# Optimization experiments

Measured on AMD Instinct MI355X. Metric: run time of the kernel, lower is better.

The kernel has to match this reference:

```python
import jax, jax.numpy as jnp
import numpy as np

B, S, H = 4, 8192, 768
NH, HD = 12, 64          # num_heads, head_size
M = 64                   # projection_dim = min(256, HD)
EPS = 1e-6

def setup_inputs() -> dict:
    key = jax.random.key(0)
    ks = jax.random.split(key, 10)
    scale_w = 0.02
    scale_p = 1.0 / np.sqrt(HD)
    return {
        'hidden_states': jax.random.normal(ks[0], (B, S, H), jnp.float32),
        'Wq': jax.random.normal(ks[1], (H, H), jnp.float32) * scale_w,
        'bq': jnp.zeros((H,), jnp.float32),
        'Wk': jax.random.normal(ks[2], (H, H), jnp.float32) * scale_w,
        'bk': jnp.zeros((H,), jnp.float32),
        'Wv': jax.random.normal(ks[3], (H, H), jnp.float32) * scale_w,
        'bv': jnp.zeros((H,), jnp.float32),
        'Wo': jax.random.normal(ks[4], (H, H), jnp.float32) * scale_w,
        'bo': jnp.zeros((H,), jnp.float32),
        'projection_matrix': jax.random.normal(ks[5], (NH, HD, M), jnp.float32) * scale_p,
    }

def reference(hidden_states, Wq, bq, Wk, bk, Wv, bv, Wo, bo, projection_matrix):
    b, s, h = hidden_states.shape
    def heads(x):  # [b,s,h] -> [b,nh,s,hd]
        return x.reshape(b, s, NH, HD).transpose(0, 2, 1, 3)
    q = heads(hidden_states @ Wq + bq)
    k = heads(hidden_states @ Wk + bk)
    v = heads(hidden_states @ Wv + bv)
    # random-feature projection + stabilized exp feature map
    qp = jnp.einsum('bhnd,hdm->bhnm', q, projection_matrix)
    kp = jnp.einsum('bhnd,hdm->bhnm', k, projection_matrix)
    qp = jnp.exp(qp - jnp.max(qp, axis=-1, keepdims=True))
    kp = jnp.exp(kp - jnp.max(kp, axis=-1, keepdims=True))
    # O(n) linear attention: kv summary [b,h,m,hd]
    kv = jnp.einsum('bhnm,bhnd->bhmd', kp, v)
    qkv = jnp.einsum('bhnm,bhmd->bhnd', qp, kv)
    k_sum = jnp.sum(kp, axis=2)                      # [b,h,m]
    normalizer = jnp.einsum('bhnm,bhm->bhn', qp, k_sum)[..., None]
    ctx = qkv / (normalizer + EPS)
    ctx = ctx.transpose(0, 2, 1, 3).reshape(b, s, NH * HD)
    return ctx @ Wo + bo
```

## Files before the change

kernel.cpp:

```cpp
#include <hip/hip_runtime.h>
#include <hip/hip_bf16.h>


#define S_    8192
#define H_    768
#define NH_   12
#define EPS_  1e-6f

typedef unsigned short U16;
typedef short bf16x8 __attribute__((ext_vector_type(8)));
typedef float f32x4  __attribute__((ext_vector_type(4)));

__device__ __forceinline__ U16 f2b(float x) {
  unsigned u = __float_as_uint(x);
  return (U16)((u + 0x7fffu + ((u >> 16) & 1u)) >> 16);
}
__device__ __forceinline__ float b2f(U16 h) {
  return __uint_as_float(((unsigned)h) << 16);
}
__device__ __forceinline__ void gl2lds16(const void* g, void* l) {
  __builtin_amdgcn_global_load_lds(
      (const __attribute__((address_space(1))) void*)g,
      (__attribute__((address_space(3))) void*)l, 16, 0, 0);
}

__global__ void zero_f32(float* __restrict__ p, int n) {
  int i = blockIdx.x * 256 + threadIdx.x;
  if (i < n) p[i] = 0.f;
}

__global__ void cvt_f32_bf16(const float* __restrict__ src, U16* __restrict__ hi, int n4) {
  int i = blockIdx.x * 256 + threadIdx.x;
  if (i >= n4) return;
  float4 x = ((const float4*)src)[i];
  ushort4 h;
  h.x = f2b(x.x); h.y = f2b(x.y); h.z = f2b(x.z); h.w = f2b(x.w);
  ((ushort4*)hi)[i] = h;
}

__global__ void fold_proj(const float* __restrict__ Wq, const float* __restrict__ bq,
                          const float* __restrict__ Wk, const float* __restrict__ bk,
                          const float* __restrict__ P,
                          float* __restrict__ Wqp, float* __restrict__ bqp,
                          float* __restrict__ Wkp, float* __restrict__ bkp) {
  __shared__ float Pl[64 * 64];
  __shared__ float WL[4 * 64];
  int h = blockIdx.y, kc = blockIdx.x, tid = threadIdx.x;
  const float* W  = blockIdx.z ? Wk : Wq;
  const float* bb = blockIdx.z ? bk : bq;
  float* Wout = blockIdx.z ? Wkp : Wqp;
  float* bout = blockIdx.z ? bkp : bqp;
  const float4* P4 = (const float4*)(P + (size_t)h * 4096);
#pragma unroll
  for (int i = 0; i < 4; ++i) ((float4*)Pl)[tid + i * 256] = P4[tid + i * 256];
  WL[tid] = W[(size_t)(kc * 4 + (tid >> 6)) * H_ + h * 64 + (tid & 63)];
  __syncthreads();
  int kl = tid >> 6, m = tid & 63;
  float acc = 0.f;
#pragma unroll
  for (int d = 0; d < 64; ++d) acc += WL[kl * 64 + d] * Pl[d * 64 + m];
  Wout[(size_t)(kc * 4 + kl) * H_ + h * 64 + m] = acc;
  if (kc == 0 && tid < 64) {
    float a2 = 0.f;
    for (int d = 0; d < 64; ++d) a2 += bb[h * 64 + d] * Pl[d * 64 + tid];
    bout[h * 64 + tid] = a2;
  }
}

__global__ void build_cat_t(const float* __restrict__ Wqp, const float* __restrict__ Wkp,
                            const float* __restrict__ Wv,  const float* __restrict__ Wo,
                            U16* __restrict__ WcatH, U16* __restrict__ WoTH) {
  __shared__ float T[64][68];
  const int kb = blockIdx.x, rb = blockIdx.y, mat = blockIdx.z;
  const int tid = threadIdx.x;
  const float* W = mat == 0 ? Wqp : (mat == 1 ? Wkp : (mat == 2 ? Wv : Wo));
#pragma unroll
  for (int p = 0; p < 4; ++p) {
    int idx = tid + p * 256;
    int rr = idx >> 4, c4 = (idx & 15) * 4;
    float4 v = *(const float4*)&W[(size_t)(kb * 64 + rr) * H_ + rb * 64 + c4];
    T[rr][c4] = v.x; T[rr][c4 + 1] = v.y; T[rr][c4 + 2] = v.z; T[rr][c4 + 3] = v.w;
  }
  __syncthreads();
  U16* dst = mat == 3 ? WoTH : WcatH;
  const int rbase = (mat == 3 ? 0 : mat * 768) + rb * 64;
#pragma unroll
  for (int p = 0; p < 4; ++p) {
    int idx = tid + p * 256;
    int r2 = idx >> 4, c2 = (idx & 15) * 4;
    ushort4 o;
    o.x = f2b(T[c2 + 0][r2]); o.y = f2b(T[c2 + 1][r2]);
    o.z = f2b(T[c2 + 2][r2]); o.w = f2b(T[c2 + 3][r2]);
    *(ushort4*)&dst[(size_t)(rbase + r2) * H_ + kb * 64 + c2] = o;
  }
}

__global__ void build_bias(const float* __restrict__ bqp, const float* __restrict__ bkp,
                           const float* __restrict__ bv, float* __restrict__ biasC) {
  int i = blockIdx.x * 256 + threadIdx.x;
  if (i >= 2304) return;
  biasC[i] = i < 768 ? bqp[i] : (i < 1536 ? bkp[i - 768] : bv[i - 1536]);
}

__global__ __launch_bounds__(256, 2) void gemm_qkv(
    const U16* __restrict__ Ahi, const U16* __restrict__ Bhi,
    const float* __restrict__ bias,
    U16* __restrict__ qp, U16* __restrict__ kpT, U16* __restrict__ vT,
    float* __restrict__ ksumF) {
  __shared__ __align__(16) U16 Us[32768];
  const int tid = threadIdx.x, w = tid >> 6, lane = tid & 63;
  const int quad = lane >> 4, l16 = lane & 15;
  const int b = blockIdx.x;
  const int mt = b & 255, nt0 = b >> 8;
  const int rowA0 = mt * 128;
  const int wm = w & 1, wn = w >> 1;
  const U16* srcA[4];
  int rowBl[4];
  unsigned ldsc[4];
  const int kch = ((lane & 7) ^ (lane >> 3)) * 8;
#pragma unroll
  for (int t = 0; t < 4; ++t) {
    int c = w * 4 + t;
    int row = c * 8 + (lane >> 3);
    srcA[t] = Ahi + (size_t)(rowA0 + row) * H_ + kch;
    rowBl[t] = row;
    ldsc[t] = (unsigned)c * 512;
  }
  auto stage = [&](int jn, int tn, int bi) {
    const int colB = (nt0 + 2 * jn) * 128;
    unsigned ub = (unsigned)bi * 16384u;
#pragma unroll
    for (int t = 0; t < 4; ++t) {
      gl2lds16(srcA[t] + tn * 64, &Us[ub + ldsc[t]]);
      gl2lds16(Bhi + (size_t)(colB + rowBl[t]) * H_ + tn * 64 + kch,
               &Us[ub + 8192u + ldsc[t]]);
    }
  };

  stage(0, 0, 0);
  for (int jj = 0; jj < 9; ++jj) {
    const int colB0 = (nt0 + 2 * jj) * 128;
    f32x4 acc[4][4] = {};
    for (int t = 0; t < 12; ++t) {
      const bool more = !(jj == 8 && t == 11);
      if (more) {
        if (t < 11) stage(jj, t + 1, (t + 1) & 1);
        else        stage(jj + 1, 0, 0);
        asm volatile("s_waitcnt vmcnt(8)" ::: "memory");
      } else {
        asm volatile("s_waitcnt vmcnt(0)" ::: "memory");
      }
      __builtin_amdgcn_sched_barrier(0);
      __builtin_amdgcn_s_barrier();
      __builtin_amdgcn_sched_barrier(0);
      const unsigned ab = (unsigned)(t & 1) * 16384u;
      bf16x8 ah[4][2], bh[4][2];
#pragma unroll
      for (int i = 0; i < 4; ++i)
#pragma unroll
        for (int ks = 0; ks < 2; ++ks)
          ah[i][ks] = *(const bf16x8*)&Us[ab +
              (unsigned)((wm * 64 + i * 16 + l16) * 64 +
                         (((ks * 4 + quad) ^ (l16 & 7)) * 8))];
#pragma unroll
      for (int j = 0; j < 4; ++j)
#pragma unroll
        for (int ks = 0; ks < 2; ++ks)
          bh[j][ks] = *(const bf16x8*)&Us[ab + 8192u +
              (unsigned)((wn * 64 + j * 16 + l16) * 64 +
                         (((ks * 4 + quad) ^ (l16 & 7)) * 8))];
      asm volatile("s_waitcnt lgkmcnt(0)" ::: "memory");
      __builtin_amdgcn_sched_barrier(0);
      __builtin_amdgcn_s_setprio(1);
#pragma unroll
      for (int ks = 0; ks < 2; ++ks)
#pragma unroll
        for (int j = 0; j < 4; ++j)
#pragma unroll
          for (int i = 0; i < 4; ++i)
            acc[i][j] = __builtin_amdgcn_mfma_f32_16x16x32_bf16(
                ah[i][ks], bh[j][ks], acc[i][j], 0, 0, 0);
      __builtin_amdgcn_s_setprio(0);
      __builtin_amdgcn_sched_barrier(0);
      __builtin_amdgcn_s_barrier();
      __builtin_amdgcn_sched_barrier(0);
    }
    const int col64 = colB0 + wn * 64;
    float bj[4];
#pragma unroll
    for (int j = 0; j < 4; ++j) bj[j] = bias[col64 + j * 16 + l16];
    if (col64 < 768) {
      const int h = col64 >> 6;
#pragma unroll
      for (int i = 0; i < 4; ++i) {
#pragma unroll
        for (int r = 0; r < 4; ++r) {
          int row = rowA0 + wm * 64 + i * 16 + quad * 4 + r;
          float v0 = acc[i][0][r] + bj[0], v1 = acc[i][1][r] + bj[1];
          float v2 = acc[i][2][r] + bj[2], v3 = acc[i][3][r] + bj[3];
          float mx = fmaxf(fmaxf(v0, v1), fmaxf(v2, v3));
          mx = fmaxf(mx, __shfl_xor(mx, 1));
          mx = fmaxf(mx, __shfl_xor(mx, 2));
          mx = fmaxf(mx, __shfl_xor(mx, 4));
          mx = fmaxf(mx, __shfl_xor(mx, 8));
          int bb = row >> 13, s = row & 8191;
          size_t base = ((size_t)(bb * NH_ + h) * S_ + s) * 64 + l16;
          qp[base +  0] = f2b(__expf(v0 - mx));
          qp[base + 16] = f2b(__expf(v1 - mx));
          qp[base + 32] = f2b(__expf(v2 - mx));
          qp[base + 48] = f2b(__expf(v3 - mx));
        }
      }
    } else {
      const int isv = col64 >= 1536;
      const int h = (col64 - (isv ? 1536 : 768)) >> 6;
      U16* dstT = isv ? vT : kpT;
      const int bh2 = (rowA0 >> 13) * NH_ + h;
      float pk[4] = {0.f, 0.f, 0.f, 0.f};
#pragma unroll
      for (int i = 0; i < 4; ++i) {
        float er[4][4];
#pragma unroll
        for (int r = 0; r < 4; ++r) {
          float v0 = acc[i][0][r] + bj[0], v1 = acc[i][1][r] + bj[1];
          float v2 = acc[i][2][r] + bj[2], v3 = acc[i][3][r] + bj[3];
          if (!isv) {
            float mx = fmaxf(fmaxf(v0, v1), fmaxf(v2, v3));
            mx = fmaxf(mx, __shfl_xor(mx, 1));
            mx = fmaxf(mx, __shfl_xor(mx, 2));
            mx = fmaxf(mx, __shfl_xor(mx, 4));
            mx = fmaxf(mx, __shfl_xor(mx, 8));
            v0 = __expf(v0 - mx); v1 = __expf(v1 - mx);
            v2 = __expf(v2 - mx); v3 = __expf(v3 - mx);
          }
          er[0][r] = v0; er[1][r] = v1; er[2][r] = v2; er[3][r] = v3;
        }
        if (!isv) {
#pragma unroll
          for (int j = 0; j < 4; ++j)
            pk[j] += er[j][0] + er[j][1] + er[j][2] + er[j][3];
        }
        int n = rowA0 + wm * 64 + i * 16 + quad * 4;
        int s = n & 8191;
#pragma unroll
        for (int j = 0; j < 4; ++j) {
          ushort4 o;
          o.x = f2b(er[j][0]); o.y = f2b(er[j][1]);
          o.z = f2b(er[j][2]); o.w = f2b(er[j][3]);
          *(ushort4*)&dstT[((size_t)bh2 * 64 + j * 16 + l16) * S_ + s] = o;
        }
      }
      if (!isv) {
#pragma unroll
        for (int j = 0; j < 4; ++j) {
          pk[j] += __shfl_xor(pk[j], 16);
          pk[j] += __shfl_xor(pk[j], 32);
        }
        if (quad == 0) {
#pragma unroll
          for (int j = 0; j < 4; ++j)
            atomicAdd(&ksumF[bh2 * 64 + j * 16 + l16], pk[j]);
        }
      }
    }
  }
}

__global__ __launch_bounds__(256, 4) void kv_accum_mfma(
    const U16* __restrict__ kpT, const U16* __restrict__ vT,
    float* __restrict__ kvM) {
  __shared__ __align__(16) U16 Us[2 * 64 * 64];
  const int tid = threadIdx.x, w = tid >> 6, lane = tid & 63;
  const int quad = lane >> 4, l16 = lane & 15;
  const int bh = blockIdx.y;
  const int n0 = blockIdx.x * 512;
  const U16* srcs[4];
  unsigned ldsoff[4];
#pragma unroll
  for (int t = 0; t < 4; ++t) {
    int c = w * 4 + t, buf = c >> 3;
    int r = (c & 7) * 8 + (lane >> 3);
    const U16* base = buf ? kpT : vT;
    srcs[t] = base + ((size_t)bh * 64 + r) * S_ + n0 + (lane & 7) * 8;
    ldsoff[t] = buf * 4096 + (c & 7) * 512;
  }
  f32x4 acc[4] = {};
  for (int nc = 0; nc < 512; nc += 64) {
#pragma unroll
    for (int t = 0; t < 4; ++t) gl2lds16(srcs[t] + nc, &Us[ldsoff[t]]);
    __syncthreads();
#pragma unroll
    for (int k0 = 0; k0 < 64; k0 += 32) {
      bf16x8 av = *(const bf16x8*)&Us[(w * 16 + l16) * 64 + k0 + quad * 8];
#pragma unroll
      for (int j = 0; j < 4; ++j) {
        bf16x8 bk = *(const bf16x8*)&Us[4096 + (j * 16 + l16) * 64 + k0 + quad * 8];
        acc[j] = __builtin_amdgcn_mfma_f32_16x16x32_bf16(av, bk, acc[j], 0, 0, 0);
      }
    }
    __syncthreads();
  }
#pragma unroll
  for (int j = 0; j < 4; ++j)
#pragma unroll
    for (int r = 0; r < 4; ++r)
      atomicAdd(&kvM[((size_t)bh * 64 + j * 16 + l16) * 64 + w * 16 + quad * 4 + r],
                acc[j][r]);
}

__global__ __launch_bounds__(256) void wkv_build(
    const float* __restrict__ kvM, const U16* __restrict__ WoTH,
    U16* __restrict__ WKVT) {
  __shared__ float kvL[64][65];
  __shared__ U16  WoL[128][66];
  const int tid = threadIdx.x;
  const int cB = blockIdx.x * 128, bh = blockIdx.y;
  const int b = bh / NH_, h = bh - b * NH_;
#pragma unroll
  for (int p = 0; p < 16; ++p) {
    int idx = tid + p * 256;
    kvL[idx >> 6][idx & 63] = kvM[(size_t)bh * 4096 + idx];
  }
#pragma unroll
  for (int p = 0; p < 32; ++p) {
    int idx = tid + p * 256;
    WoL[idx >> 6][idx & 63] = WoTH[(size_t)(cB + (idx >> 6)) * H_ + h * 64 + (idx & 63)];
  }
  __syncthreads();
  const int c = tid & 127, m0 = (tid >> 7) * 32;
  float acc[32] = {};
  for (int d = 0; d < 64; ++d) {
    float wv = b2f(WoL[c][d]);
#pragma unroll
    for (int mm = 0; mm < 32; ++mm) acc[mm] += wv * kvL[m0 + mm][d];
  }
  U16* dst = WKVT + (size_t)b * 589824 + (size_t)(cB + c) * H_ + h * 64 + m0;
#pragma unroll
  for (int mm = 0; mm < 32; mm += 4) {
    ushort4 o;
    o.x = f2b(acc[mm]); o.y = f2b(acc[mm + 1]);
    o.z = f2b(acc[mm + 2]); o.w = f2b(acc[mm + 3]);
    *(ushort4*)&dst[mm] = o;
  }
}

__global__ __launch_bounds__(256) void qpn_scale(
    U16* __restrict__ qp, const float* __restrict__ ksumF) {
  __shared__ float ks[64];
  const int tid = threadIdx.x;
  const int bh = blockIdx.y, s0 = blockIdx.x * 64;
  if (tid < 64) ks[tid] = ksumF[bh * 64 + tid];
  __syncthreads();
  const int row = tid >> 2, q = tid & 3;
  size_t src = ((size_t)bh * S_ + s0 + row) * 64 + q * 16;
  bf16x8 x0 = *(const bf16x8*)&qp[src];
  bf16x8 x1 = *(const bf16x8*)&qp[src + 8];
  float f[16];
  float n = 0.f;
#pragma unroll
  for (int e = 0; e < 8; ++e) {
    f[e] = b2f((U16)x0[e]);     n += f[e] * ks[q * 16 + e];
    f[e + 8] = b2f((U16)x1[e]); n += f[e + 8] * ks[q * 16 + 8 + e];
  }
  n += __shfl_xor(n, 1);
  n += __shfl_xor(n, 2);
  const float inv = 1.f / (n + EPS_);
#pragma unroll
  for (int g = 0; g < 4; ++g) {
    ushort4 o;
    o.x = f2b(f[g * 4 + 0] * inv); o.y = f2b(f[g * 4 + 1] * inv);
    o.z = f2b(f[g * 4 + 2] * inv); o.w = f2b(f[g * 4 + 3] * inv);
    *(ushort4*)&qp[src + g * 4] = o;
  }
}

__global__ __launch_bounds__(256, 2) void out_gemm(
    const U16* __restrict__ qpn, const U16* __restrict__ WKVT,
    const float* __restrict__ bo, float* __restrict__ out) {
  __shared__ __align__(16) U16 Us[32768];
  const int tid = threadIdx.x, w = tid >> 6, lane = tid & 63;
  const int quad = lane >> 4, l16 = lane & 15;
  const int b = blockIdx.x;
  const int mt = b & 255, nt0 = b >> 8;
  const int rowA0 = mt * 128;
  const int batch = mt >> 6, s0 = (mt & 63) * 128;
  const int bh0 = batch * NH_;
  const int wm = w & 1, wn = w >> 1;
  const int kch = ((lane & 7) ^ (lane >> 3)) * 8;
  int rowc[4];
  unsigned ldsc[4];
#pragma unroll
  for (int t = 0; t < 4; ++t) {
    rowc[t] = (w * 4 + t) * 8 + (lane >> 3);
    ldsc[t] = (unsigned)(w * 4 + t) * 512;
  }
  const U16* wb = WKVT + (size_t)batch * 589824;
  auto stage = [&](int jn, int tn, int bi) {
    const int colB = (nt0 * 3 + jn) * 128;
    unsigned ub = (unsigned)bi * 16384u;
    const U16* abase = qpn + ((size_t)(bh0 + tn) * S_ + s0) * 64 + kch;
    const U16* bbase = wb + (size_t)colB * H_ + tn * 64 + kch;
#pragma unroll
    for (int t = 0; t < 4; ++t) {
      gl2lds16(abase + rowc[t] * 64, &Us[ub + ldsc[t]]);
      gl2lds16(bbase + (size_t)rowc[t] * H_, &Us[ub + 8192u + ldsc[t]]);
    }
  };

  stage(0, 0, 0);
  for (int jj = 0; jj < 3; ++jj) {
    const int colB0 = (nt0 * 3 + jj) * 128;
    f32x4 acc[4][4] = {};
    for (int t = 0; t < 12; ++t) {
      const bool more = !(jj == 2 && t == 11);
      if (more) {
        if (t < 11) stage(jj, t + 1, (t + 1) & 1);
        else        stage(jj + 1, 0, 0);
        asm volatile("s_waitcnt vmcnt(8)" ::: "memory");
      } else {
        asm volatile("s_waitcnt vmcnt(0)" ::: "memory");
      }
      __builtin_amdgcn_sched_barrier(0);
      __builtin_amdgcn_s_barrier();
      __builtin_amdgcn_sched_barrier(0);
      const unsigned ab = (unsigned)(t & 1) * 16384u;
      bf16x8 ah[4][2], bh[4][2];
#pragma unroll
      for (int i = 0; i < 4; ++i)
#pragma unroll
        for (int ks = 0; ks < 2; ++ks)
          ah[i][ks] = *(const bf16x8*)&Us[ab +
              (unsigned)((wm * 64 + i * 16 + l16) * 64 +
                         (((ks * 4 + quad) ^ (l16 & 7)) * 8))];
#pragma unroll
      for (int j = 0; j < 4; ++j)
#pragma unroll
        for (int ks = 0; ks < 2; ++ks)
          bh[j][ks] = *(const bf16x8*)&Us[ab + 8192u +
              (unsigned)((wn * 64 + j * 16 + l16) * 64 +
                         (((ks * 4 + quad) ^ (l16 & 7)) * 8))];
      asm volatile("s_waitcnt lgkmcnt(0)" ::: "memory");
      __builtin_amdgcn_sched_barrier(0);
      __builtin_amdgcn_s_setprio(1);
#pragma unroll
      for (int ks = 0; ks < 2; ++ks)
#pragma unroll
        for (int j = 0; j < 4; ++j)
#pragma unroll
          for (int i = 0; i < 4; ++i)
            acc[i][j] = __builtin_amdgcn_mfma_f32_16x16x32_bf16(
                ah[i][ks], bh[j][ks], acc[i][j], 0, 0, 0);
      __builtin_amdgcn_s_setprio(0);
      __builtin_amdgcn_sched_barrier(0);
      __builtin_amdgcn_s_barrier();
      __builtin_amdgcn_sched_barrier(0);
    }
#pragma unroll
    for (int i = 0; i < 4; ++i) {
      int row = rowA0 + wm * 64 + i * 16 + quad * 4;
#pragma unroll
      for (int j = 0; j < 4; ++j) {
        int col = colB0 + wn * 64 + j * 16 + l16;
        float bvv = bo[col];
#pragma unroll
        for (int r = 0; r < 4; ++r)
          out[(size_t)(row + r) * H_ + col] = acc[i][j][r] + bvv;
      }
    }
  }
}

extern "C" void kernel_launch(void* const* d_in, const int* in_sizes, int n_in,
                              void* d_out, int out_size, void* d_ws, size_t ws_size,
                              hipStream_t stream) {
  const float* hs = (const float*)d_in[0];
  const float* Wq = (const float*)d_in[1];
  const float* bq = (const float*)d_in[2];
  const float* Wk = (const float*)d_in[3];
  const float* bk = (const float*)d_in[4];
  const float* Wv = (const float*)d_in[5];
  const float* bv = (const float*)d_in[6];
  const float* Wo = (const float*)d_in[7];
  const float* bo = (const float*)d_in[8];
  const float* P  = (const float*)d_in[9];
  float* out = (float*)d_out;

  char* ws = (char*)d_ws;
  size_t off = 0;
  auto alloc = [&](size_t bytes) -> void* {
    void* p = ws + off;
    off = (off + bytes + 255) & ~(size_t)255;
    return p;
  };
  U16*   hs_hi = (U16*)alloc(50331648);
  float* WqpF  = (float*)alloc(2359296);
  float* WkpF  = (float*)alloc(2359296);
  float* bqpF  = (float*)alloc(3072);
  float* bkpF  = (float*)alloc(3072);
  U16*   WcatH = (U16*)alloc(3538944);
  U16*   WoTH  = (U16*)alloc(1179648);
  float* biasC = (float*)alloc(9216);
  U16*   qp    = (U16*)alloc(50331648);
  U16*   kpT   = (U16*)alloc(50331648);
  U16*   vT    = (U16*)alloc(50331648);
  float* kvM   = (float*)alloc(786432);
  float* ksumF = (float*)alloc(12288);
  U16*   WKVT  = (U16*)alloc(4718592);

  zero_f32<<<dim3(780), dim3(256), 0, stream>>>(kvM, 199680);
  cvt_f32_bf16<<<dim3(24576), dim3(256), 0, stream>>>(hs, hs_hi, 6291456);
  fold_proj<<<dim3(192, 12, 2), dim3(256), 0, stream>>>(Wq, bq, Wk, bk, P, WqpF, bqpF, WkpF, bkpF);
  build_cat_t<<<dim3(12, 12, 4), dim3(256), 0, stream>>>(WqpF, WkpF, Wv, Wo, WcatH, WoTH);
  build_bias<<<dim3(9), dim3(256), 0, stream>>>(bqpF, bkpF, bv, biasC);
  gemm_qkv<<<dim3(512), dim3(256), 0, stream>>>(hs_hi, WcatH, biasC, qp, kpT, vT, ksumF);
  kv_accum_mfma<<<dim3(16, 48), dim3(256), 0, stream>>>(kpT, vT, kvM);
  wkv_build<<<dim3(6, 48), dim3(256), 0, stream>>>(kvM, WoTH, WKVT);
  qpn_scale<<<dim3(128, 48), dim3(256), 0, stream>>>(qp, ksumF);
  out_gemm<<<dim3(512), dim3(256), 0, stream>>>(qp, WKVT, bo, out);
}
```

Baseline: 518.6 us.

## Fuse prologue kernels and merge kv accumulation, Wkv build, and q normalization

Merges zeroing, bf16 conversion, projection folding, weight transposes and bias assembly into a single prologue kernel, with the folded Q/K projection written directly as transposed bf16. Combines kv accumulation, the Wo·kv build and q normalization into one kernel, using a per-head atomic ticket so the last block of each head builds the fused output weight. This removes several launches and an fp32 intermediate, but the Wkv build now runs on only one block per head, which reduces its parallelism.

```diff
diff --git a/kernel.cpp b/kernel.cpp
--- a/kernel.cpp
+++ b/kernel.cpp
@@ -24,66 +24,84 @@
       (__attribute__((address_space(3))) void*)l, 16, 0, 0);
 }
 
-__global__ void zero_f32(float* __restrict__ p, int n) {
-  int i = blockIdx.x * 256 + threadIdx.x;
-  if (i < n) p[i] = 0.f;
-}
-
-__global__ void cvt_f32_bf16(const float* __restrict__ src, U16* __restrict__ hi, int n4) {
-  int i = blockIdx.x * 256 + threadIdx.x;
-  if (i >= n4) return;
-  float4 x = ((const float4*)src)[i];
-  ushort4 h;
-  h.x = f2b(x.x); h.y = f2b(x.y); h.z = f2b(x.z); h.w = f2b(x.w);
-  ((ushort4*)hi)[i] = h;
-}
-
-__global__ void fold_proj(const float* __restrict__ Wq, const float* __restrict__ bq,
-                          const float* __restrict__ Wk, const float* __restrict__ bk,
-                          const float* __restrict__ P,
-                          float* __restrict__ Wqp, float* __restrict__ bqp,
-                          float* __restrict__ Wkp, float* __restrict__ bkp) {
-  __shared__ float Pl[64 * 64];
-  __shared__ float WL[4 * 64];
-  int h = blockIdx.y, kc = blockIdx.x, tid = threadIdx.x;
-  const float* W  = blockIdx.z ? Wk : Wq;
-  const float* bb = blockIdx.z ? bk : bq;
-  float* Wout = blockIdx.z ? Wkp : Wqp;
-  float* bout = blockIdx.z ? bkp : bqp;
-  const float4* P4 = (const float4*)(P + (size_t)h * 4096);
-#pragma unroll
-  for (int i = 0; i < 4; ++i) ((float4*)Pl)[tid + i * 256] = P4[tid + i * 256];
-  WL[tid] = W[(size_t)(kc * 4 + (tid >> 6)) * H_ + h * 64 + (tid & 63)];
-  __syncthreads();
-  int kl = tid >> 6, m = tid & 63;
-  float acc = 0.f;
-#pragma unroll
-  for (int d = 0; d < 64; ++d) acc += WL[kl * 64 + d] * Pl[d * 64 + m];
-  Wout[(size_t)(kc * 4 + kl) * H_ + h * 64 + m] = acc;
-  if (kc == 0 && tid < 64) {
-    float a2 = 0.f;
-    for (int d = 0; d < 64; ++d) a2 += bb[h * 64 + d] * Pl[d * 64 + tid];
-    bout[h * 64 + tid] = a2;
-  }
-}
-
-__global__ void build_cat_t(const float* __restrict__ Wqp, const float* __restrict__ Wkp,
-                            const float* __restrict__ Wv,  const float* __restrict__ Wo,
-                            U16* __restrict__ WcatH, U16* __restrict__ WoTH) {
-  __shared__ float T[64][68];
-  const int kb = blockIdx.x, rb = blockIdx.y, mat = blockIdx.z;
-  const int tid = threadIdx.x;
-  const float* W = mat == 0 ? Wqp : (mat == 1 ? Wkp : (mat == 2 ? Wv : Wo));
+__global__ __launch_bounds__(256) void prologue(
+    const float* __restrict__ hs, const float* __restrict__ Wq,
+    const float* __restrict__ bq, const float* __restrict__ Wk,
+    const float* __restrict__ bk, const float* __restrict__ Wv,
+    const float* __restrict__ bv, const float* __restrict__ Wo,
+    const float* __restrict__ P,
+    U16* __restrict__ hs_hi, U16* __restrict__ WcatH, U16* __restrict__ WoTH,
+    float* __restrict__ biasC, float* __restrict__ zbase) {
+  __shared__ float sm[8192];
+  const int bid = blockIdx.x, tid = threadIdx.x;
+  if (bid < 781) {
+    int i = bid * 256 + tid;
+    if (i < 199728) zbase[i] = 0.f;
+    return;
+  }
+  if (bid < 25357) {
+    int i = (bid - 781) * 256 + tid;
+    float4 x = ((const float4*)hs)[i];
+    ushort4 h;
+    h.x = f2b(x.x); h.y = f2b(x.y); h.z = f2b(x.z); h.w = f2b(x.w);
+    ((ushort4*)hs_hi)[i] = h;
+    return;
+  }
+  if (bid < 25645) {
+    int f = bid - 25357;
+    int z = f / 144, rem = f - z * 144, h = rem / 12, kcB = rem - (rem / 12) * 12;
+    float* Pl = sm;
+    float* WL = sm + 4096;
+    const float* W = z ? Wk : Wq;
+    const float4* P4 = (const float4*)(P + (size_t)h * 4096);
+#pragma unroll
+    for (int p = 0; p < 4; ++p) ((float4*)Pl)[tid + p * 256] = P4[tid + p * 256];
+#pragma unroll
+    for (int p = 0; p < 4; ++p) {
+      int idx = tid + p * 256;
+      int kk = idx >> 4, d4 = (idx & 15) * 4;
+      *(float4*)&WL[kk * 64 + d4] =
+          *(const float4*)&W[(size_t)(kcB * 64 + kk) * H_ + h * 64 + d4];
+    }
+    __syncthreads();
+    const int m = tid & 63, kg = tid >> 6;
+    float acc[16] = {};
+    for (int d = 0; d < 64; ++d) {
+      float pv = Pl[d * 64 + m];
+#pragma unroll
+      for (int k2 = 0; k2 < 16; ++k2) acc[k2] += WL[(kg * 16 + k2) * 64 + d] * pv;
+    }
+    U16* dst = WcatH + (size_t)(z * 768 + h * 64 + m) * H_ + kcB * 64 + kg * 16;
+#pragma unroll
+    for (int k2 = 0; k2 < 16; k2 += 4) {
+      ushort4 o;
+      o.x = f2b(acc[k2]); o.y = f2b(acc[k2 + 1]);
+      o.z = f2b(acc[k2 + 2]); o.w = f2b(acc[k2 + 3]);
+      *(ushort4*)&dst[k2] = o;
+    }
+    if (kcB == 0 && tid < 64) {
+      const float* bb = z ? bk : bq;
+      float a2 = 0.f;
+      for (int d = 0; d < 64; ++d) a2 += bb[h * 64 + d] * Pl[d * 64 + tid];
+      biasC[z * 768 + h * 64 + tid] = a2;
+    }
+    return;
+  }
+  const int isWo = bid >= 25789;
+  int v = bid - (isWo ? 25789 : 25645);
+  int kb = v / 12, rb = v - kb * 12;
+  const float* W = isWo ? Wo : Wv;
+  float (*T)[68] = (float(*)[68])sm;
 #pragma unroll
   for (int p = 0; p < 4; ++p) {
     int idx = tid + p * 256;
     int rr = idx >> 4, c4 = (idx & 15) * 4;
-    float4 v = *(const float4*)&W[(size_t)(kb * 64 + rr) * H_ + rb * 64 + c4];
-    T[rr][c4] = v.x; T[rr][c4 + 1] = v.y; T[rr][c4 + 2] = v.z; T[rr][c4 + 3] = v.w;
+    float4 x = *(const float4*)&W[(size_t)(kb * 64 + rr) * H_ + rb * 64 + c4];
+    T[rr][c4] = x.x; T[rr][c4 + 1] = x.y; T[rr][c4 + 2] = x.z; T[rr][c4 + 3] = x.w;
   }
   __syncthreads();
-  U16* dst = mat == 3 ? WoTH : WcatH;
-  const int rbase = (mat == 3 ? 0 : mat * 768) + rb * 64;
+  U16* dst = isWo ? WoTH : WcatH;
+  const int rbase = (isWo ? 0 : 1536) + rb * 64;
 #pragma unroll
   for (int p = 0; p < 4; ++p) {
     int idx = tid + p * 256;
@@ -93,13 +111,10 @@
     o.z = f2b(T[c2 + 2][r2]); o.w = f2b(T[c2 + 3][r2]);
     *(ushort4*)&dst[(size_t)(rbase + r2) * H_ + kb * 64 + c2] = o;
   }
-}
-
-__global__ void build_bias(const float* __restrict__ bqp, const float* __restrict__ bkp,
-                           const float* __restrict__ bv, float* __restrict__ biasC) {
-  int i = blockIdx.x * 256 + threadIdx.x;
-  if (i >= 2304) return;
-  biasC[i] = i < 768 ? bqp[i] : (i < 1536 ? bkp[i - 768] : bv[i - 1536]);
+  if (!isWo && kb == 0 && rb == 0) {
+#pragma unroll
+    for (int p = 0; p < 3; ++p) biasC[1536 + tid + p * 256] = bv[tid + p * 256];
+  }
 }
 
 __global__ __launch_bounds__(256, 2) void gemm_qkv(
@@ -266,89 +281,103 @@
   }
 }
 
-__global__ __launch_bounds__(256, 4) void kv_accum_mfma(
+__global__ __launch_bounds__(256, 2) void kv_qpn(
     const U16* __restrict__ kpT, const U16* __restrict__ vT,
-    float* __restrict__ kvM) {
-  __shared__ __align__(16) U16 Us[2 * 64 * 64];
-  const int tid = threadIdx.x, w = tid >> 6, lane = tid & 63;
-  const int quad = lane >> 4, l16 = lane & 15;
-  const int bh = blockIdx.y;
-  const int n0 = blockIdx.x * 512;
-  const U16* srcs[4];
-  unsigned ldsoff[4];
-#pragma unroll
-  for (int t = 0; t < 4; ++t) {
-    int c = w * 4 + t, buf = c >> 3;
-    int r = (c & 7) * 8 + (lane >> 3);
-    const U16* base = buf ? kpT : vT;
-    srcs[t] = base + ((size_t)bh * 64 + r) * S_ + n0 + (lane & 7) * 8;
-    ldsoff[t] = buf * 4096 + (c & 7) * 512;
-  }
-  f32x4 acc[4] = {};
-  for (int nc = 0; nc < 512; nc += 64) {
-#pragma unroll
-    for (int t = 0; t < 4; ++t) gl2lds16(srcs[t] + nc, &Us[ldsoff[t]]);
+    float* __restrict__ kvM, const float* __restrict__ ksumF,
+    unsigned* __restrict__ tick, const U16* __restrict__ WoTH,
+    U16* __restrict__ WKVT, U16* __restrict__ qp) {
+  __shared__ __align__(16) U16 Us[8192];
+  __shared__ int lastf;
+  const int bid = blockIdx.x, tid = threadIdx.x;
+  if (bid < 768) {
+    const int w = tid >> 6, lane = tid & 63;
+    const int quad = lane >> 4, l16 = lane & 15;
+    const int bh = bid >> 4;
+    const int n0 = (bid & 15) * 512;
+    const U16* srcs[4];
+    unsigned ldsoff[4];
+#pragma unroll
+    for (int t = 0; t < 4; ++t) {
+      int c = w * 4 + t, buf = c >> 3;
+      int r = (c & 7) * 8 + (lane >> 3);
+      const U16* base = buf ? kpT : vT;
+      srcs[t] = base + ((size_t)bh * 64 + r) * S_ + n0 + (lane & 7) * 8;
+      ldsoff[t] = buf * 4096 + (c & 7) * 512;
+    }
+    f32x4 acc[4] = {};
+    for (int nc = 0; nc < 512; nc += 64) {
+#pragma unroll
+      for (int t = 0; t < 4; ++t) gl2lds16(srcs[t] + nc, &Us[ldsoff[t]]);
+      __syncthreads();
+#pragma unroll
+      for (int k0 = 0; k0 < 64; k0 += 32) {
+        bf16x8 av = *(const bf16x8*)&Us[(w * 16 + l16) * 64 + k0 + quad * 8];
+#pragma unroll
+        for (int j = 0; j < 4; ++j) {
+          bf16x8 bk = *(const bf16x8*)&Us[4096 + (j * 16 + l16) * 64 + k0 + quad * 8];
+          acc[j] = __builtin_amdgcn_mfma_f32_16x16x32_bf16(av, bk, acc[j], 0, 0, 0);
+        }
+      }
+      __syncthreads();
+    }
+#pragma unroll
+    for (int j = 0; j < 4; ++j)
+#pragma unroll
+      for (int r = 0; r < 4; ++r)
+        atomicAdd(&kvM[((size_t)bh * 64 + j * 16 + l16) * 64 + w * 16 + quad * 4 + r],
+                  acc[j][r]);
+    __threadfence();
     __syncthreads();
-#pragma unroll
-    for (int k0 = 0; k0 < 64; k0 += 32) {
-      bf16x8 av = *(const bf16x8*)&Us[(w * 16 + l16) * 64 + k0 + quad * 8];
-#pragma unroll
-      for (int j = 0; j < 4; ++j) {
-        bf16x8 bk = *(const bf16x8*)&Us[4096 + (j * 16 + l16) * 64 + k0 + quad * 8];
-        acc[j] = __builtin_amdgcn_mfma_f32_16x16x32_bf16(av, bk, acc[j], 0, 0, 0);
-      }
-    }
+    if (tid == 0) lastf = (atomicAdd(&tick[bh], 1u) == 15u) ? 1 : 0;
     __syncthreads();
-  }
-#pragma unroll
-  for (int j = 0; j < 4; ++j)
-#pragma unroll
-    for (int r = 0; r < 4; ++r)
-      atomicAdd(&kvM[((size_t)bh * 64 + j * 16 + l16) * 64 + w * 16 + quad * 4 + r],
-                acc[j][r]);
-}
-
-__global__ __launch_bounds__(256) void wkv_build(
-    const float* __restrict__ kvM, const U16* __restrict__ WoTH,
-    U16* __restrict__ WKVT) {
-  __shared__ float kvL[64][65];
-  __shared__ U16  WoL[128][66];
-  const int tid = threadIdx.x;
-  const int cB = blockIdx.x * 128, bh = blockIdx.y;
-  const int b = bh / NH_, h = bh - b * NH_;
-#pragma unroll
-  for (int p = 0; p < 16; ++p) {
-    int idx = tid + p * 256;
-    kvL[idx >> 6][idx & 63] = kvM[(size_t)bh * 4096 + idx];
-  }
-#pragma unroll
-  for (int p = 0; p < 32; ++p) {
-    int idx = tid + p * 256;
-    WoL[idx >> 6][idx & 63] = WoTH[(size_t)(cB + (idx >> 6)) * H_ + h * 64 + (idx & 63)];
-  }
-  __syncthreads();
-  const int c = tid & 127, m0 = (tid >> 7) * 32;
-  float acc[32] = {};
-  for (int d = 0; d < 64; ++d) {
-    float wv = b2f(WoL[c][d]);
-#pragma unroll
-    for (int mm = 0; mm < 32; ++mm) acc[mm] += wv * kvL[m0 + mm][d];
-  }
-  U16* dst = WKVT + (size_t)b * 589824 + (size_t)(cB + c) * H_ + h * 64 + m0;
-#pragma unroll
-  for (int mm = 0; mm < 32; mm += 4) {
-    ushort4 o;
-    o.x = f2b(acc[mm]); o.y = f2b(acc[mm + 1]);
-    o.z = f2b(acc[mm + 2]); o.w = f2b(acc[mm + 3]);
-    *(ushort4*)&dst[mm] = o;
-  }
-}
-
-__global__ __launch_bounds__(256) void qpn_scale(
-    U16* __restrict__ qp, const float* __restrict__ ksumF) {
-  __shared__ float ks[64];
-  const int tid = threadIdx.x;
-  const int bh = blockIdx.y, s0 = blockIdx.x * 64;
+    if (!lastf) return;
+    __threadfence();
+    float* kvL = (float*)Us;
+#pragma unroll
+    for (int p = 0; p < 16; ++p) {
+      int i = tid + p * 256;
+      kvL[i] = kvM[(size_t)bh * 4096 + i];
+    }
+    __syncthreads();
+    const int b = bh / NH_, h = bh - b * NH_;
+    for (int cc = 0; cc < 3; ++cc) {
+      int c = tid + cc * 256;
+      const U16* wr = WoTH + (size_t)c * H_ + h * 64;
+#pragma unroll
+      for (int mc = 0; mc < 4; ++mc) {
+        float a16[16] = {};
+#pragma unroll
+        for (int dg = 0; dg < 4; ++dg) {
+          ushort4 w0 = *(const ushort4*)&wr[dg * 16 + 0];
+          ushort4 w1 = *(const ushort4*)&wr[dg * 16 + 4];
+          ushort4 w2 = *(const ushort4*)&wr[dg * 16 + 8];
+          ushort4 w3 = *(const ushort4*)&wr[dg * 16 + 12];
+          U16 wv16[16] = {w0.x, w0.y, w0.z, w0.w, w1.x, w1.y, w1.z, w1.w,
+                          w2.x, w2.y, w2.z, w2.w, w3.x, w3.y, w3.z, w3.w};
+#pragma unroll
+          for (int dd = 0; dd < 16; ++dd) {
+            float wv = b2f(wv16[dd]);
+            int d = dg * 16 + dd;
+#pragma unroll
+            for (int mm = 0; mm < 16; ++mm)
+              a16[mm] += wv * kvL[(mc * 16 + mm) * 64 + d];
+          }
+        }
+        U16* dst = WKVT + (size_t)b * 589824 + (size_t)c * H_ + h * 64 + mc * 16;
+#pragma unroll
+        for (int mm = 0; mm < 16; mm += 4) {
+          ushort4 o;
+          o.x = f2b(a16[mm]); o.y = f2b(a16[mm + 1]);
+          o.z = f2b(a16[mm + 2]); o.w = f2b(a16[mm + 3]);
+          *(ushort4*)&dst[mm] = o;
+        }
+      }
+    }
+    return;
+  }
+  const int qid = bid - 768;
+  const int bh = qid >> 7, s0 = (qid & 127) * 64;
+  float* ks = (float*)Us;
   if (tid < 64) ks[tid] = ksumF[bh * 64 + tid];
   __syncthreads();
   const int row = tid >> 2, q = tid & 3;
@@ -493,10 +522,6 @@
     return p;
   };
   U16*   hs_hi = (U16*)alloc(50331648);
-  float* WqpF  = (float*)alloc(2359296);
-  float* WkpF  = (float*)alloc(2359296);
-  float* bqpF  = (float*)alloc(3072);
-  float* bkpF  = (float*)alloc(3072);
   U16*   WcatH = (U16*)alloc(3538944);
   U16*   WoTH  = (U16*)alloc(1179648);
   float* biasC = (float*)alloc(9216);
@@ -505,16 +530,12 @@
   U16*   vT    = (U16*)alloc(50331648);
   float* kvM   = (float*)alloc(786432);
   float* ksumF = (float*)alloc(12288);
+  unsigned* tick = (unsigned*)alloc(192);
   U16*   WKVT  = (U16*)alloc(4718592);
 
-  zero_f32<<<dim3(780), dim3(256), 0, stream>>>(kvM, 199680);
-  cvt_f32_bf16<<<dim3(24576), dim3(256), 0, stream>>>(hs, hs_hi, 6291456);
-  fold_proj<<<dim3(192, 12, 2), dim3(256), 0, stream>>>(Wq, bq, Wk, bk, P, WqpF, bqpF, WkpF, bkpF);
-  build_cat_t<<<dim3(12, 12, 4), dim3(256), 0, stream>>>(WqpF, WkpF, Wv, Wo, WcatH, WoTH);
-  build_bias<<<dim3(9), dim3(256), 0, stream>>>(bqpF, bkpF, bv, biasC);
+  prologue<<<dim3(25933), dim3(256), 0, stream>>>(
+      hs, Wq, bq, Wk, bk, Wv, bv, Wo, P, hs_hi, WcatH, WoTH, biasC, kvM);
   gemm_qkv<<<dim3(512), dim3(256), 0, stream>>>(hs_hi, WcatH, biasC, qp, kpT, vT, ksumF);
-  kv_accum_mfma<<<dim3(16, 48), dim3(256), 0, stream>>>(kpT, vT, kvM);
-  wkv_build<<<dim3(6, 48), dim3(256), 0, stream>>>(kvM, WoTH, WKVT);
-  qpn_scale<<<dim3(128, 48), dim3(256), 0, stream>>>(qp, ksumF);
+  kv_qpn<<<dim3(6912), dim3(256), 0, stream>>>(kpT, vT, kvM, ksumF, tick, WoTH, WKVT, qp);
   out_gemm<<<dim3(512), dim3(256), 0, stream>>>(qp, WKVT, bo, out);
 }
```

After: 927.0 us. 1.79x slower.
